# Performance work log

Measured on AMD Instinct MI355X. Metric: run time of the kernel, lower is better.

Reference implementation:

```python
import jax, jax.numpy as jnp
import numpy as np

B, Nc, Ns, Nz, Nx, K = 2, 128, 2048, 256, 256, 4


def setup_inputs() -> dict:
    key = jax.random.key(0)
    k1, k2, k3 = jax.random.split(key, 3)
    # RF channel data: [B, Nc, Ns, K]
    rf = jax.random.normal(k1, (B, Nc, Ns, K), dtype=jnp.float32)
    # Imaging grid point coordinates (meters), ~4 cm field: [B, Nz, Nx, 3]
    g = jax.random.uniform(k2, (B, Nz, Nx, 3), dtype=jnp.float32) * 0.04
    # Receiver element positions (meters): [B, Nc, 3]
    pr = jax.random.uniform(k3, (B, Nc, 3), dtype=jnp.float32) * 0.04
    # Acquisition params per batch: [c0 (m/s), fs (Hz), t0 (s), unused]
    p = jnp.tile(jnp.array([1540.0, 40.0e6, 0.0, 0.0], dtype=jnp.float32), (B, 1))
    return {"rf": rf, "g": g, "pr": pr, "p": p}


def reference(rf, g, pr, p):
    # rf: [B, Nc, Ns, K]; g: [B, Nz, Nx, 3]; pr: [B, Nc, 3]; p: [B, 4]
    b, nc, ns, k = rf.shape
    nz, nx = g.shape[1], g.shape[2]
    m = nz * nx

    c0 = p[:, 0][:, None, None, None]
    fs = p[:, 1][:, None, None, None]
    t0 = p[:, 2][:, None, None, None]

    d_tx = g[..., 2]  # [B, Nz, Nx] transmit path = depth coordinate
    # receive path: distance from each receiver to each pixel -> [B, Nc, Nz, Nx]
    d_rx = jnp.linalg.norm(g[:, None, :, :, :] - pr[:, :, None, None, :], axis=-1)
    # fractional sample index of the round-trip delay
    samples = fs * (t0 + (d_rx + d_tx[:, None, :, :])) / c0  # [B, Nc, Nz, Nx]
    s = samples.reshape(b, nc, m)

    # batch_interp_regular_1d_grid with x_ref_min=0, x_ref_max=Ns-1 on Ns points
    # -> unit grid spacing, constant extension (clamp) outside the grid.
    s = jnp.clip(s, 0.0, float(ns - 1))
    i0 = jnp.clip(jnp.floor(s).astype(jnp.int32), 0, ns - 2)  # [B, Nc, M]
    w = (s - i0.astype(s.dtype))[..., None]                   # [B, Nc, M, 1]

    idx0 = jnp.broadcast_to(i0[..., None], (b, nc, m, k))
    y0 = jnp.take_along_axis(rf, idx0, axis=2)      # [B, Nc, M, K]
    y1 = jnp.take_along_axis(rf, idx0 + 1, axis=2)  # [B, Nc, M, K]
    interp = y0 * (1.0 - w) + y1 * w

    # delay-and-sum over channels, then back to image layout [B, Nz, Nx, K]
    y_das = jnp.sum(interp, axis=1).reshape(b, nz, nx, k)
    return y_das
```

## Files before the change

kernel.cpp:

```cpp
#include <hip/hip_runtime.h>
#include <hip/hip_fp16.h>


#define NBATCH 2
#define NC 128
#define NS 2048
#define NK 4
#define NM 65536

#define THREADS 1024
#define PX_PER_THREAD 2
#define PX_PER_BLOCK (THREADS * PX_PER_THREAD)
#define C_PER_BLOCK 32
#define N_CHUNKS (NC / C_PER_BLOCK)
#define N_TILES (NM / PX_PER_BLOCK)
#define NBLOCKS (NBATCH * N_TILES * N_CHUNKS)

#define PART_BYTES ((size_t)N_CHUNKS * NBATCH * NM * NK * 4)

typedef float f32x4 __attribute__((ext_vector_type(4)));

__device__ __forceinline__ uint4 cvt8(float4 a, float4 b) {
    const __half2 h0 = __floats2half2_rn(a.x, a.y);
    const __half2 h1 = __floats2half2_rn(a.z, a.w);
    const __half2 h2 = __floats2half2_rn(b.x, b.y);
    const __half2 h3 = __floats2half2_rn(b.z, b.w);
    return make_uint4(__builtin_bit_cast(unsigned, h0),
                      __builtin_bit_cast(unsigned, h1),
                      __builtin_bit_cast(unsigned, h2),
                      __builtin_bit_cast(unsigned, h3));
}

template <bool ATOMIC>
__global__ __launch_bounds__(THREADS, 4) void das_kernel(
    const float* __restrict__ rf, const float* __restrict__ g,
    const float* __restrict__ pr, const float* __restrict__ p,
    float* __restrict__ dst)
{
    __shared__ uint4 sbuf[2][NS / 2];

    const int bid   = blockIdx.x;
    const int chunk = bid & (N_CHUNKS - 1);
    const int tile  = (bid >> 2) & (N_TILES - 1);
    const int b     = bid >> 7;
    const int t     = threadIdx.x;
    const int px0   = tile * PX_PER_BLOCK;

    const float c0v = p[b * 4 + 0];
    const float fsv = p[b * 4 + 1];
    const float t0v = p[b * 4 + 2];
    const float scale = fsv / c0v;
    const float sb0   = scale * t0v;

    float gx[PX_PER_THREAD], gy[PX_PER_THREAD], gzv[PX_PER_THREAD],
          sbase[PX_PER_THREAD];
#pragma unroll
    for (int j = 0; j < PX_PER_THREAD; ++j) {
        const int m = px0 + j * THREADS + t;
        const float* gp = g + ((size_t)b * NM + m) * 3;
        gx[j]  = gp[0];
        gy[j]  = gp[1];
        gzv[j] = gp[2];
        sbase[j] = fmaf(scale, gzv[j], sb0);
    }

    float4 acc[PX_PER_THREAD];
#pragma unroll
    for (int j = 0; j < PX_PER_THREAD; ++j) acc[j] = make_float4(0.f, 0.f, 0.f, 0.f);

    const int ch0 = chunk * C_PER_BLOCK;
    const float* slice0 = rf + (size_t)(b * NC + ch0) * NS * NK;

    {
        const float4* s4 = (const float4*)slice0;
        const float4 a0 = s4[2 * t];
        const float4 a1 = s4[2 * t + 1];
        sbuf[0][t] = cvt8(a0, a1);
    }

    for (int cc = 0; cc < C_PER_BLOCK; ++cc) {
        __syncthreads();

        float4 a0, a1;
        if (cc + 1 < C_PER_BLOCK) {
            const float4* s4 = (const float4*)(slice0 + (size_t)(cc + 1) * NS * NK);
            a0 = s4[2 * t];
            a1 = s4[2 * t + 1];
        }

        const uint2* lb = (const uint2*)&sbuf[cc & 1][0];
        const float* prp = pr + ((size_t)(b * NC + ch0 + cc)) * 3;
        const float prx = prp[0], pry = prp[1], prz = prp[2];

#pragma unroll
        for (int j = 0; j < PX_PER_THREAD; ++j) {
            const float dx = gx[j]  - prx;
            const float dy = gy[j]  - pry;
            const float dz = gzv[j] - prz;
            const float drx = __builtin_amdgcn_sqrtf(fmaf(dx, dx, fmaf(dy, dy, dz * dz)));
            float s = fmaf(scale, drx, sbase[j]);
            s = fminf(fmaxf(s, 0.0f), (float)(NS - 1));
            const float fi = fminf(floorf(s), (float)(NS - 2));
            const float w  = s - fi;
            const float wm = 1.0f - w;
            const int i0 = (int)fi;
            const uint2 u0 = lb[i0];
            const uint2 u1 = lb[i0 + 1];
            const float2 y0a = __half22float2(__builtin_bit_cast(__half2, u0.x));
            const float2 y0b = __half22float2(__builtin_bit_cast(__half2, u0.y));
            const float2 y1a = __half22float2(__builtin_bit_cast(__half2, u1.x));
            const float2 y1b = __half22float2(__builtin_bit_cast(__half2, u1.y));
            acc[j].x = fmaf(y0a.x, wm, fmaf(y1a.x, w, acc[j].x));
            acc[j].y = fmaf(y0a.y, wm, fmaf(y1a.y, w, acc[j].y));
            acc[j].z = fmaf(y0b.x, wm, fmaf(y1b.x, w, acc[j].z));
            acc[j].w = fmaf(y0b.y, wm, fmaf(y1b.y, w, acc[j].w));
        }

        if (cc + 1 < C_PER_BLOCK)
            sbuf[(cc + 1) & 1][t] = cvt8(a0, a1);
    }

    if (ATOMIC) {
        float* ob = dst + (size_t)b * NM * NK;
#pragma unroll
        for (int j = 0; j < PX_PER_THREAD; ++j) {
            const int m = px0 + j * THREADS + t;
            float* op = ob + (size_t)m * NK;
            atomicAdd(op + 0, acc[j].x);
            atomicAdd(op + 1, acc[j].y);
            atomicAdd(op + 2, acc[j].z);
            atomicAdd(op + 3, acc[j].w);
        }
    } else {
        f32x4* pw = (f32x4*)dst + (size_t)(chunk * NBATCH + b) * NM;
#pragma unroll
        for (int j = 0; j < PX_PER_THREAD; ++j) {
            const int m = px0 + j * THREADS + t;
            const f32x4 v = {acc[j].x, acc[j].y, acc[j].z, acc[j].w};
            __builtin_nontemporal_store(v, pw + m);
        }
    }
}

__global__ __launch_bounds__(256) void reduce_kernel(
    const f32x4* __restrict__ part, f32x4* __restrict__ out)
{
    const int i = blockIdx.x * 256 + threadIdx.x;
    const size_t stride = (size_t)NBATCH * NM;
    f32x4 a = __builtin_nontemporal_load(part + i);
#pragma unroll
    for (int c = 1; c < N_CHUNKS; ++c) {
        const f32x4 v = __builtin_nontemporal_load(part + c * stride + i);
        a += v;
    }
    out[i] = a;
}

extern "C" void kernel_launch(void* const* d_in, const int* in_sizes, int n_in,
                              void* d_out, int out_size, void* d_ws, size_t ws_size,
                              hipStream_t stream) {
    (void)in_sizes; (void)n_in;
    const float* rf = (const float*)d_in[0];
    const float* g  = (const float*)d_in[1];
    const float* pr = (const float*)d_in[2];
    const float* p  = (const float*)d_in[3];
    float* out = (float*)d_out;

    if (ws_size >= PART_BYTES) {
        das_kernel<false><<<NBLOCKS, THREADS, 0, stream>>>(rf, g, pr, p, (float*)d_ws);
        reduce_kernel<<<(NBATCH * NM) / 256, 256, 0, stream>>>((const f32x4*)d_ws,
                                                               (f32x4*)out);
    } else {
        (void)hipMemsetAsync(d_out, 0, (size_t)out_size * sizeof(float), stream);
        das_kernel<true><<<NBLOCKS, THREADS, 0, stream>>>(rf, g, pr, p, out);
    }
}
```

Baseline: 91.78 us.

## Fuse channel-chunk reduction into DAS kernel via last-block counter

Removes the separate reduce kernel. Each block writes its partial sums, then bumps a per-tile atomic counter, and the last block for a tile sums the other chunks' partials and writes the output. Tiling also changes to 4 pixels per thread with 16 channels per block, giving 8 chunks and 16 tiles. This trades a second kernel launch and a full partial reread for a memset, threadfences and a tail reduction done by a subset of blocks, with more register pressure per thread.

After: 245.0 us. +166.9%, slower.

```diff
diff --git a/kernel.cpp b/kernel.cpp
--- a/kernel.cpp
+++ b/kernel.cpp
@@ -9,14 +9,15 @@
 #define NM 65536
 
 #define THREADS 1024
-#define PX_PER_THREAD 2
+#define PX_PER_THREAD 4
 #define PX_PER_BLOCK (THREADS * PX_PER_THREAD)
-#define C_PER_BLOCK 32
+#define C_PER_BLOCK 16
 #define N_CHUNKS (NC / C_PER_BLOCK)
 #define N_TILES (NM / PX_PER_BLOCK)
 #define NBLOCKS (NBATCH * N_TILES * N_CHUNKS)
 
 #define PART_BYTES ((size_t)N_CHUNKS * NBATCH * NM * NK * 4)
+#define CNT_BYTES ((size_t)NBATCH * N_TILES * 4)
 
 typedef float f32x4 __attribute__((ext_vector_type(4)));
 
@@ -35,13 +36,15 @@
 __global__ __launch_bounds__(THREADS, 4) void das_kernel(
     const float* __restrict__ rf, const float* __restrict__ g,
     const float* __restrict__ pr, const float* __restrict__ p,
-    float* __restrict__ dst)
+    float* __restrict__ part, unsigned* __restrict__ cnt,
+    float* __restrict__ out)
 {
     __shared__ uint4 sbuf[2][NS / 2];
+    __shared__ int s_rank;
 
     const int bid   = blockIdx.x;
     const int chunk = bid & (N_CHUNKS - 1);
-    const int tile  = (bid >> 2) & (N_TILES - 1);
+    const int tile  = (bid >> 3) & (N_TILES - 1);
     const int b     = bid >> 7;
     const int t     = threadIdx.x;
     const int px0   = tile * PX_PER_BLOCK;
@@ -121,7 +124,7 @@
     }
 
     if (ATOMIC) {
-        float* ob = dst + (size_t)b * NM * NK;
+        float* ob = out + (size_t)b * NM * NK;
 #pragma unroll
         for (int j = 0; j < PX_PER_THREAD; ++j) {
             const int m = px0 + j * THREADS + t;
@@ -131,29 +134,39 @@
             atomicAdd(op + 2, acc[j].z);
             atomicAdd(op + 3, acc[j].w);
         }
-    } else {
-        f32x4* pw = (f32x4*)dst + (size_t)(chunk * NBATCH + b) * NM;
+        return;
+    }
+
+    f32x4* pw = (f32x4*)part + (size_t)(chunk * NBATCH + b) * NM;
+#pragma unroll
+    for (int j = 0; j < PX_PER_THREAD; ++j) {
+        const int m = px0 + j * THREADS + t;
+        const f32x4 v = {acc[j].x, acc[j].y, acc[j].z, acc[j].w};
+        pw[m] = v;
+    }
+
+    __threadfence();
+    __syncthreads();
+    if (t == 0) s_rank = (int)atomicAdd(&cnt[b * N_TILES + tile], 1u);
+    __syncthreads();
+
+    if (s_rank == N_CHUNKS - 1) {
+        __threadfence();
+        const f32x4* pp = (const f32x4*)part;
+        f32x4* ob = (f32x4*)out + (size_t)b * NM;
 #pragma unroll
         for (int j = 0; j < PX_PER_THREAD; ++j) {
             const int m = px0 + j * THREADS + t;
-            const f32x4 v = {acc[j].x, acc[j].y, acc[j].z, acc[j].w};
-            __builtin_nontemporal_store(v, pw + m);
+            f32x4 s = {acc[j].x, acc[j].y, acc[j].z, acc[j].w};
+#pragma unroll
+            for (int c = 0; c < N_CHUNKS; ++c) {
+                if (c == 0 && chunk == 0) continue;
+                if (c != chunk)
+                    s += pp[(size_t)(c * NBATCH + b) * NM + m];
+            }
+            ob[m] = s;
         }
     }
-}
-
-__global__ __launch_bounds__(256) void reduce_kernel(
-    const f32x4* __restrict__ part, f32x4* __restrict__ out)
-{
-    const int i = blockIdx.x * 256 + threadIdx.x;
-    const size_t stride = (size_t)NBATCH * NM;
-    f32x4 a = __builtin_nontemporal_load(part + i);
-#pragma unroll
-    for (int c = 1; c < N_CHUNKS; ++c) {
-        const f32x4 v = __builtin_nontemporal_load(part + c * stride + i);
-        a += v;
-    }
-    out[i] = a;
 }
 
 extern "C" void kernel_launch(void* const* d_in, const int* in_sizes, int n_in,
@@ -166,12 +179,14 @@
     const float* p  = (const float*)d_in[3];
     float* out = (float*)d_out;
 
-    if (ws_size >= PART_BYTES) {
-        das_kernel<false><<<NBLOCKS, THREADS, 0, stream>>>(rf, g, pr, p, (float*)d_ws);
-        reduce_kernel<<<(NBATCH * NM) / 256, 256, 0, stream>>>((const f32x4*)d_ws,
-                                                               (f32x4*)out);
+    if (ws_size >= PART_BYTES + CNT_BYTES) {
+        unsigned* cnt = (unsigned*)((char*)d_ws + PART_BYTES);
+        (void)hipMemsetAsync(cnt, 0, CNT_BYTES, stream);
+        das_kernel<false><<<NBLOCKS, THREADS, 0, stream>>>(
+            rf, g, pr, p, (float*)d_ws, cnt, out);
     } else {
         (void)hipMemsetAsync(d_out, 0, (size_t)out_size * sizeof(float), stream);
-        das_kernel<true><<<NBLOCKS, THREADS, 0, stream>>>(rf, g, pr, p, out);
+        das_kernel<true><<<NBLOCKS, THREADS, 0, stream>>>(
+            rf, g, pr, p, nullptr, nullptr, out);
     }
 }
```
